# Performance work log

Measured on AMD Instinct MI355X. Metric: run time of the kernel, lower is better.

## Reference

```python
import jax, jax.numpy as jnp
import numpy as np

EMBED_DIM = 1024
NUM_HEADS = 16
HEAD_DIM = EMBED_DIM // NUM_HEADS
SCALE = HEAD_DIM ** -0.5


def setup_inputs() -> dict:
    key = jax.random.key(0)
    k_x, k_qkv_w, k_qkv_b, k_p_w, k_p_b = jax.random.split(key, 5)
    B, N, C = 4, 2048, EMBED_DIM
    std = C ** -0.5
    return {
        "x": jax.random.normal(k_x, (B, N, C), dtype=jnp.float32),
        "qkv_w": jax.random.normal(k_qkv_w, (C, 3 * C), dtype=jnp.float32) * std,
        "qkv_b": jax.random.normal(k_qkv_b, (3 * C,), dtype=jnp.float32) * 0.02,
        "proj_w": jax.random.normal(k_p_w, (C, C), dtype=jnp.float32) * std,
        "proj_b": jax.random.normal(k_p_b, (C,), dtype=jnp.float32) * 0.02,
    }


def reference(x, qkv_w, qkv_b, proj_w, proj_b):
    B, N, C = x.shape
    H, D = NUM_HEADS, HEAD_DIM
    # fused QKV projection: [B, N, 3C] -> [3, B, H, N, D]
    qkv = (x @ qkv_w + qkv_b).reshape(B, N, 3, H, D).transpose(2, 0, 3, 1, 4)
    q, k, v = qkv[0], qkv[1], qkv[2]
    # explicit N x N attention (faithful to the original, no fused SDPA)
    attn = jnp.einsum("bhqd,bhkd->bhqk", q, k) * SCALE
    attn = jax.nn.softmax(attn, axis=-1)
    out = jnp.einsum("bhqk,bhkd->bhqd", attn, v)  # [B, H, N, D]
    out = out.transpose(0, 2, 1, 3).reshape(B, N, C)
    return out @ proj_w + proj_b
```

## Files before the change

### kernel.cpp

```cpp
#include <hip/hip_runtime.h>
#include <hip/hip_bf16.h>

typedef __bf16 bf16x8 __attribute__((ext_vector_type(8)));
typedef __bf16 bf16x4 __attribute__((ext_vector_type(4)));
typedef float  f32x4  __attribute__((ext_vector_type(4)));

#define MFMA_BF16(a, b, c) __builtin_amdgcn_mfma_f32_16x16x32_bf16((a), (b), (c), 0, 0, 0)

typedef const __attribute__((address_space(1))) void* gas_ptr;
typedef __attribute__((address_space(3))) void* las_ptr;

__device__ __forceinline__ void gload_lds16(const void* g, void* l) {
    __builtin_amdgcn_global_load_lds((gas_ptr)g, (las_ptr)l, 16, 0, 0);
}

#define LOG2E 1.44269504088896f
#define QSCALE 0.1803368801111204f

__global__ __launch_bounds__(256) void cvt_f32_bf16(const float* __restrict__ in,
                                                    __bf16* __restrict__ out, int n4) {
    int i = blockIdx.x * 256 + threadIdx.x;
    if (i < n4) {
        float4 v = ((const float4*)in)[i];
        bf16x4 o = {(__bf16)v.x, (__bf16)v.y, (__bf16)v.z, (__bf16)v.w};
        ((bf16x4*)out)[i] = o;
    }
}

__global__ __launch_bounds__(256) void transpose_cvt(const float* __restrict__ in,
                                                     __bf16* __restrict__ out, int R, int C) {
    __shared__ float t[32][33];
    int bx = blockIdx.x * 32, by = blockIdx.y * 32;
    int x = bx + threadIdx.x;
    for (int j = threadIdx.y; j < 32; j += 8)
        t[j][threadIdx.x] = in[(size_t)(by + j) * C + x];
    __syncthreads();
    int x2 = by + threadIdx.x;
    for (int j = threadIdx.y; j < 32; j += 8)
        out[(size_t)(bx + j) * R + x2] = (__bf16)t[threadIdx.x][j];
}

template <int MODE>
__global__ __launch_bounds__(256) void gemm_bt(const __bf16* __restrict__ A,
                                               const __bf16* __restrict__ Bt,
                                               const float* __restrict__ bias,
                                               float* __restrict__ outp,
                                               __bf16* __restrict__ Qp,
                                               __bf16* __restrict__ Kp,
                                               __bf16* __restrict__ Vp,
                                               int M, int Nn, int K) {
    __shared__ __align__(16) __bf16 As[128 * 32];
    __shared__ __align__(16) __bf16 Bs[128 * 32];
    const int tid = threadIdx.x, lane = tid & 63, w = tid >> 6;
    const int wr = w >> 1, wc = w & 1;
    const int row0 = blockIdx.y * 128, col0 = blockIdx.x * 128;
    const __bf16* Ag = A + (size_t)row0 * K;
    const __bf16* Bg = Bt + (size_t)col0 * K;
    const int lr = lane >> 2;
    const int lk = (lane & 3) * 8;
    const int frow = lane & 15, fq = lane >> 4;
    f32x4 acc[4][4];
    for (int i = 0; i < 4; ++i)
        for (int j = 0; j < 4; ++j) acc[i][j] = (f32x4)0.f;

    for (int k0 = 0; k0 < K; k0 += 32) {
        __syncthreads();
        for (int it = 0; it < 2; ++it) {
            int ci = 2 * w + it;
            gload_lds16(Ag + (size_t)(ci * 16 + lr) * K + k0 + lk, &As[ci * 512]);
            gload_lds16(Bg + (size_t)(ci * 16 + lr) * K + k0 + lk, &Bs[ci * 512]);
        }
        __syncthreads();
        bf16x8 af[4], bf[4];
        for (int i = 0; i < 4; ++i)
            af[i] = *(const bf16x8*)&As[(wr * 64 + i * 16 + frow) * 32 + fq * 8];
        for (int j = 0; j < 4; ++j)
            bf[j] = *(const bf16x8*)&Bs[(wc * 64 + j * 16 + frow) * 32 + fq * 8];
        for (int i = 0; i < 4; ++i)
            for (int j = 0; j < 4; ++j) acc[i][j] = MFMA_BF16(af[i], bf[j], acc[i][j]);
    }

    for (int i = 0; i < 4; ++i) {
        int rbase = row0 + wr * 64 + i * 16 + fq * 4;
        for (int j = 0; j < 4; ++j) {
            int c = col0 + wc * 64 + j * 16 + frow;
            float bv = bias[c];
            if (MODE == 0) {
                int which = c >> 10;
                int h = (c >> 6) & 15;
                int d = c & 63;
                if (which == 2) {
                    int b = rbase >> 11, n = rbase & 2047;
                    bf16x4 vv = {(__bf16)(acc[i][j][0] + bv), (__bf16)(acc[i][j][1] + bv),
                                 (__bf16)(acc[i][j][2] + bv), (__bf16)(acc[i][j][3] + bv)};
                    *(bf16x4*)&Vp[(size_t)(((b << 4) + h) * 64 + d) * 2048 + n] = vv;
                } else {
                    for (int rg = 0; rg < 4; ++rg) {
                        int rr = rbase + rg;
                        int b = rr >> 11, n = rr & 2047;
                        float v = acc[i][j][rg] + bv;
                        if (which == 0)
                            Qp[(size_t)(((b << 4) + h) * 2048 + n) * 64 + d] =
                                (__bf16)(v * QSCALE);
                        else
                            Kp[(size_t)(((b << 4) + h) * 2048 + n) * 64 + d] = (__bf16)v;
                    }
                }
            } else {
                for (int rg = 0; rg < 4; ++rg)
                    outp[(size_t)(rbase + rg) * Nn + c] = acc[i][j][rg] + bv;
            }
        }
    }
}

__global__ __launch_bounds__(256, 4) void flash_attn4(const __bf16* __restrict__ Q,
                                                      const __bf16* __restrict__ K,
                                                      const __bf16* __restrict__ Vt,
                                                      __bf16* __restrict__ O) {
    __shared__ __align__(16) __bf16 Kts[2][4096];
    __shared__ __align__(16) __bf16 Vts[2][4096];
    __shared__ __align__(16) __bf16 Ps[4][1024];
    const int tid = threadIdx.x, lane = tid & 63, w = tid >> 6;
    const int frow = lane & 15, fq = lane >> 4;
    const int bh = blockIdx.y;
    const int q0 = blockIdx.x * 128;
    const __bf16* Qg = Q + ((size_t)bh * 2048 + q0 + w * 32) * 64;
    const __bf16* Kb = K + (size_t)bh * 2048 * 64;
    const __bf16* Vb = Vt + (size_t)bh * 64 * 2048;

    bf16x8 qf[2][2];
#pragma unroll
    for (int nt = 0; nt < 2; ++nt)
#pragma unroll
        for (int ks = 0; ks < 2; ++ks)
            qf[nt][ks] = *(const bf16x8*)(Qg + (nt * 16 + frow) * 64 + ks * 32 + fq * 8);

    bf16x8 ones;
#pragma unroll
    for (int i = 0; i < 8; ++i) ones[i] = (__bf16)1.0f;

    f32x4 acc[2][4];
#pragma unroll
    for (int i = 0; i < 2; ++i)
#pragma unroll
        for (int j = 0; j < 4; ++j) acc[i][j] = (f32x4)0.f;
    f32x4 acc_l[2];
#pragma unroll
    for (int i = 0; i < 2; ++i) acc_l[i] = (f32x4)0.f;

    const int s_r16 = lane >> 2;
    const int s_c8 = (lane & 3) * 8;

    auto stage = [&](int kt, int buf) {
#pragma unroll
        for (int it = 0; it < 2; ++it) {
            int ci = 2 * w + it;
            int ks = ci >> 2;
            int r16 = (ci & 3) * 16 + s_r16;
            gload_lds16(Kb + (size_t)(kt * 64 + r16) * 64 + ks * 32 + s_c8,
                        &Kts[buf][ci * 512]);
            gload_lds16(Vb + (size_t)r16 * 2048 + kt * 64 + ks * 32 + s_c8,
                        &Vts[buf][ci * 512]);
        }
    };

    stage(0, 0);

    const int swz = frow & 3;
    const int pe = (fq ^ swz) * 8;
    __bf16* Pw = Ps[w];

    for (int kt = 0; kt < 32; ++kt) {
        const int cur = kt & 1;
        __syncthreads();
        if (kt < 31) stage(kt + 1, cur ^ 1);

        const __bf16* Kc = Kts[cur];
        const __bf16* Vc = Vts[cur];

#pragma unroll
        for (int ph = 0; ph < 2; ++ph) {
#pragma unroll
            for (int mi = 0; mi < 2; ++mi) {
                int mt = ph * 2 + mi;
                bf16x8 a0 = *(const bf16x8*)&Kc[(mt * 16 + frow) * 32 + fq * 8];
                bf16x8 a1 = *(const bf16x8*)&Kc[2048 + (mt * 16 + frow) * 32 + fq * 8];
                f32x4 s[2];
#pragma unroll
                for (int nt = 0; nt < 2; ++nt) {
                    s[nt] = MFMA_BF16(a0, qf[nt][0], (f32x4)0.f);
                    s[nt] = MFMA_BF16(a1, qf[nt][1], s[nt]);
                }
                int u = mi * 2 + (fq >> 1);
                int e = ((u ^ swz) << 3) + ((fq & 1) << 2);
#pragma unroll
                for (int nt = 0; nt < 2; ++nt) {
                    float p0 = __builtin_exp2f(s[nt][0]);
                    float p1 = __builtin_exp2f(s[nt][1]);
                    float p2 = __builtin_exp2f(s[nt][2]);
                    float p3 = __builtin_exp2f(s[nt][3]);
                    bf16x4 pk = {(__bf16)p0, (__bf16)p1, (__bf16)p2, (__bf16)p3};
                    *(bf16x4*)&Pw[(nt * 16 + frow) * 32 + e] = pk;
                }
            }

            bf16x8 vf[4];
#pragma unroll
            for (int nt = 0; nt < 4; ++nt)
                vf[nt] = *(const bf16x8*)&Vc[ph * 2048 + (nt * 16 + frow) * 32 + fq * 8];
#pragma unroll
            for (int mq = 0; mq < 2; ++mq) {
                bf16x8 p = *(const bf16x8*)&Pw[(mq * 16 + frow) * 32 + pe];
#pragma unroll
                for (int nt = 0; nt < 4; ++nt)
                    acc[mq][nt] = MFMA_BF16(p, vf[nt], acc[mq][nt]);
                acc_l[mq] = MFMA_BF16(p, ones, acc_l[mq]);
            }
        }
    }

    const int b = bh >> 4, h = bh & 15;
#pragma unroll
    for (int mq = 0; mq < 2; ++mq)
#pragma unroll
        for (int r = 0; r < 4; ++r) {
            float linv = 1.0f / acc_l[mq][r];
            int qg = q0 + w * 32 + mq * 16 + fq * 4 + r;
            __bf16* orow = O + ((size_t)(b * 2048 + qg)) * 1024 + h * 64 + frow;
#pragma unroll
            for (int nt = 0; nt < 4; ++nt)
                orow[nt * 16] = (__bf16)(acc[mq][nt][r] * linv);
        }
}

extern "C" void kernel_launch(void* const* d_in, const int* in_sizes, int n_in,
                              void* d_out, int out_size, void* d_ws, size_t ws_size,
                              hipStream_t stream) {
    const float* x      = (const float*)d_in[0];
    const float* qkv_w  = (const float*)d_in[1];
    const float* qkv_b  = (const float*)d_in[2];
    const float* proj_w = (const float*)d_in[3];
    const float* proj_b = (const float*)d_in[4];
    float* out = (float*)d_out;

    char* ws = (char*)d_ws;
    __bf16* Xb     = (__bf16*)(ws);
    __bf16* Wqkvt  = (__bf16*)(ws + 16777216);
    __bf16* Wpt    = (__bf16*)(ws + 23068672);
    __bf16* Qb     = (__bf16*)(ws + 25165824);
    __bf16* Kb     = (__bf16*)(ws + 41943040);
    __bf16* Vtb    = (__bf16*)(ws + 58720256);
    __bf16* AttnOut = Xb;

    cvt_f32_bf16<<<8192, 256, 0, stream>>>(x, Xb, 2097152);
    transpose_cvt<<<dim3(96, 32), dim3(32, 8), 0, stream>>>(qkv_w, Wqkvt, 1024, 3072);
    transpose_cvt<<<dim3(32, 32), dim3(32, 8), 0, stream>>>(proj_w, Wpt, 1024, 1024);

    gemm_bt<0><<<dim3(24, 64), 256, 0, stream>>>(Xb, Wqkvt, qkv_b, nullptr,
                                                 Qb, Kb, Vtb, 8192, 3072, 1024);

    flash_attn4<<<dim3(16, 64), 256, 0, stream>>>(Qb, Kb, Vtb, AttnOut);

    gemm_bt<1><<<dim3(8, 64), 256, 0, stream>>>(AttnOut, Wpt, proj_b, out,
                                                nullptr, nullptr, nullptr, 8192, 1024, 1024);
}
```

Measured before the change: 313.3 us.

## Rewrite attention with 32x32 MFMA and register-shuffled P instead of LDS

```diff
diff --git a/kernel.cpp b/kernel.cpp
--- a/kernel.cpp
+++ b/kernel.cpp
@@ -3,9 +3,13 @@
 
 typedef __bf16 bf16x8 __attribute__((ext_vector_type(8)));
 typedef __bf16 bf16x4 __attribute__((ext_vector_type(4)));
+typedef __bf16 bf16x2 __attribute__((ext_vector_type(2)));
 typedef float  f32x4  __attribute__((ext_vector_type(4)));
+typedef float  f32x16 __attribute__((ext_vector_type(16)));
+typedef unsigned uint4v __attribute__((ext_vector_type(4)));
 
 #define MFMA_BF16(a, b, c) __builtin_amdgcn_mfma_f32_16x16x32_bf16((a), (b), (c), 0, 0, 0)
+#define MFMA32(a, b, c) __builtin_amdgcn_mfma_f32_32x32x16_bf16((a), (b), (c), 0, 0, 0)
 
 typedef const __attribute__((address_space(1))) void* gas_ptr;
 typedef __attribute__((address_space(3))) void* las_ptr;
@@ -114,62 +118,54 @@
     }
 }
 
-__global__ __launch_bounds__(256, 4) void flash_attn4(const __bf16* __restrict__ Q,
+__global__ __launch_bounds__(256, 4) void flash_attn5(const __bf16* __restrict__ Q,
                                                       const __bf16* __restrict__ K,
                                                       const __bf16* __restrict__ Vt,
                                                       __bf16* __restrict__ O) {
     __shared__ __align__(16) __bf16 Kts[2][4096];
     __shared__ __align__(16) __bf16 Vts[2][4096];
-    __shared__ __align__(16) __bf16 Ps[4][1024];
     const int tid = threadIdx.x, lane = tid & 63, w = tid >> 6;
-    const int frow = lane & 15, fq = lane >> 4;
+    const int l31 = lane & 31, h = lane >> 5;
     const int bh = blockIdx.y;
     const int q0 = blockIdx.x * 128;
-    const __bf16* Qg = Q + ((size_t)bh * 2048 + q0 + w * 32) * 64;
     const __bf16* Kb = K + (size_t)bh * 2048 * 64;
     const __bf16* Vb = Vt + (size_t)bh * 64 * 2048;
 
-    bf16x8 qf[2][2];
-#pragma unroll
-    for (int nt = 0; nt < 2; ++nt)
-#pragma unroll
-        for (int ks = 0; ks < 2; ++ks)
-            qf[nt][ks] = *(const bf16x8*)(Qg + (nt * 16 + frow) * 64 + ks * 32 + fq * 8);
+    const __bf16* Qg = Q + ((size_t)bh * 2048 + q0 + w * 32 + l31) * 64;
+    bf16x8 qf[4];
+#pragma unroll
+    for (int c = 0; c < 4; ++c)
+        qf[c] = *(const bf16x8*)(Qg + c * 16 + h * 8);
 
     bf16x8 ones;
 #pragma unroll
     for (int i = 0; i < 8; ++i) ones[i] = (__bf16)1.0f;
 
-    f32x4 acc[2][4];
-#pragma unroll
-    for (int i = 0; i < 2; ++i)
-#pragma unroll
-        for (int j = 0; j < 4; ++j) acc[i][j] = (f32x4)0.f;
-    f32x4 acc_l[2];
-#pragma unroll
-    for (int i = 0; i < 2; ++i) acc_l[i] = (f32x4)0.f;
-
-    const int s_r16 = lane >> 2;
-    const int s_c8 = (lane & 3) * 8;
+    f32x16 acc[2];
+    acc[0] = (f32x16)0.f;
+    acc[1] = (f32x16)0.f;
+    f32x16 accl = (f32x16)0.f;
+
+    const int key = l31 & 7;
+    int koff[4];
+#pragma unroll
+    for (int c = 0; c < 4; ++c) koff[c] = ((2 * c + h) ^ key) * 8;
+    const int rbase = l31 * 64;
 
     auto stage = [&](int kt, int buf) {
 #pragma unroll
         for (int it = 0; it < 2; ++it) {
             int ci = 2 * w + it;
-            int ks = ci >> 2;
-            int r16 = (ci & 3) * 16 + s_r16;
-            gload_lds16(Kb + (size_t)(kt * 64 + r16) * 64 + ks * 32 + s_c8,
+            int rloc = ci * 8 + (lane >> 3);
+            int ulog = (lane & 7) ^ (lane >> 3);
+            gload_lds16(Kb + (size_t)(kt * 64 + rloc) * 64 + ulog * 8,
                         &Kts[buf][ci * 512]);
-            gload_lds16(Vb + (size_t)r16 * 2048 + kt * 64 + ks * 32 + s_c8,
+            gload_lds16(Vb + (size_t)rloc * 2048 + kt * 64 + ulog * 8,
                         &Vts[buf][ci * 512]);
         }
     };
 
     stage(0, 0);
-
-    const int swz = frow & 3;
-    const int pe = (fq ^ swz) * 8;
-    __bf16* Pw = Ps[w];
 
     for (int kt = 0; kt < 32; ++kt) {
         const int cur = kt & 1;
@@ -180,58 +176,50 @@
         const __bf16* Vc = Vts[cur];
 
 #pragma unroll
-        for (int ph = 0; ph < 2; ++ph) {
-#pragma unroll
-            for (int mi = 0; mi < 2; ++mi) {
-                int mt = ph * 2 + mi;
-                bf16x8 a0 = *(const bf16x8*)&Kc[(mt * 16 + frow) * 32 + fq * 8];
-                bf16x8 a1 = *(const bf16x8*)&Kc[2048 + (mt * 16 + frow) * 32 + fq * 8];
-                f32x4 s[2];
-#pragma unroll
-                for (int nt = 0; nt < 2; ++nt) {
-                    s[nt] = MFMA_BF16(a0, qf[nt][0], (f32x4)0.f);
-                    s[nt] = MFMA_BF16(a1, qf[nt][1], s[nt]);
+        for (int T = 0; T < 2; ++T) {
+            f32x16 sacc = (f32x16)0.f;
+#pragma unroll
+            for (int c = 0; c < 4; ++c) {
+                bf16x8 kf = *(const bf16x8*)&Kc[T * 2048 + rbase + koff[c]];
+                sacc = MFMA32(kf, qf[c], sacc);
+            }
+            unsigned pk[8];
+#pragma unroll
+            for (int r2 = 0; r2 < 8; ++r2) {
+                bf16x2 pp = {(__bf16)__builtin_exp2f(sacc[2 * r2]),
+                             (__bf16)__builtin_exp2f(sacc[2 * r2 + 1])};
+                pk[r2] = __builtin_bit_cast(unsigned, pp);
+            }
+#pragma unroll
+            for (int cc = 0; cc < 2; ++cc) {
+                unsigned tA = h ? pk[4 * cc] : pk[4 * cc + 2];
+                unsigned tB = h ? pk[4 * cc + 1] : pk[4 * cc + 3];
+                unsigned rA = (unsigned)__shfl_xor((int)tA, 32, 64);
+                unsigned rB = (unsigned)__shfl_xor((int)tB, 32, 64);
+                uint4v fu = {h ? rA : pk[4 * cc], h ? rB : pk[4 * cc + 1],
+                             h ? pk[4 * cc + 2] : rA, h ? pk[4 * cc + 3] : rB};
+                bf16x8 fragP = __builtin_bit_cast(bf16x8, fu);
+                const int cg = T * 2 + cc;
+#pragma unroll
+                for (int t = 0; t < 2; ++t) {
+                    bf16x8 vf = *(const bf16x8*)&Vc[t * 2048 + rbase + koff[cg]];
+                    acc[t] = MFMA32(fragP, vf, acc[t]);
                 }
-                int u = mi * 2 + (fq >> 1);
-                int e = ((u ^ swz) << 3) + ((fq & 1) << 2);
-#pragma unroll
-                for (int nt = 0; nt < 2; ++nt) {
-                    float p0 = __builtin_exp2f(s[nt][0]);
-                    float p1 = __builtin_exp2f(s[nt][1]);
-                    float p2 = __builtin_exp2f(s[nt][2]);
-                    float p3 = __builtin_exp2f(s[nt][3]);
-                    bf16x4 pk = {(__bf16)p0, (__bf16)p1, (__bf16)p2, (__bf16)p3};
-                    *(bf16x4*)&Pw[(nt * 16 + frow) * 32 + e] = pk;
-                }
-            }
-
-            bf16x8 vf[4];
-#pragma unroll
-            for (int nt = 0; nt < 4; ++nt)
-                vf[nt] = *(const bf16x8*)&Vc[ph * 2048 + (nt * 16 + frow) * 32 + fq * 8];
-#pragma unroll
-            for (int mq = 0; mq < 2; ++mq) {
-                bf16x8 p = *(const bf16x8*)&Pw[(mq * 16 + frow) * 32 + pe];
-#pragma unroll
-                for (int nt = 0; nt < 4; ++nt)
-                    acc[mq][nt] = MFMA_BF16(p, vf[nt], acc[mq][nt]);
-                acc_l[mq] = MFMA_BF16(p, ones, acc_l[mq]);
-            }
-        }
-    }
-
-    const int b = bh >> 4, h = bh & 15;
-#pragma unroll
-    for (int mq = 0; mq < 2; ++mq)
-#pragma unroll
-        for (int r = 0; r < 4; ++r) {
-            float linv = 1.0f / acc_l[mq][r];
-            int qg = q0 + w * 32 + mq * 16 + fq * 4 + r;
-            __bf16* orow = O + ((size_t)(b * 2048 + qg)) * 1024 + h * 64 + frow;
-#pragma unroll
-            for (int nt = 0; nt < 4; ++nt)
-                orow[nt * 16] = (__bf16)(acc[mq][nt][r] * linv);
-        }
+                accl = MFMA32(fragP, ones, accl);
+            }
+        }
+    }
+
+    const int b = bh >> 4, hd = bh & 15;
+#pragma unroll
+    for (int reg = 0; reg < 16; ++reg) {
+        int qloc = (reg & 3) + 8 * (reg >> 2) + 4 * h;
+        int qg = q0 + w * 32 + qloc;
+        float linv = 1.0f / accl[reg];
+        __bf16* orow = O + ((size_t)(b * 2048 + qg)) * 1024 + hd * 64;
+        orow[l31] = (__bf16)(acc[0][reg] * linv);
+        orow[32 + l31] = (__bf16)(acc[1][reg] * linv);
+    }
 }
 
 extern "C" void kernel_launch(void* const* d_in, const int* in_sizes, int n_in,
@@ -260,7 +248,7 @@
     gemm_bt<0><<<dim3(24, 64), 256, 0, stream>>>(Xb, Wqkvt, qkv_b, nullptr,
                                                  Qb, Kb, Vtb, 8192, 3072, 1024);
 
-    flash_attn4<<<dim3(16, 64), 256, 0, stream>>>(Qb, Kb, Vtb, AttnOut);
+    flash_attn5<<<dim3(16, 64), 256, 0, stream>>>(Qb, Kb, Vtb, AttnOut);
 
     gemm_bt<1><<<dim3(8, 64), 256, 0, stream>>>(AttnOut, Wpt, proj_b, out,
                                                 nullptr, nullptr, nullptr, 8192, 1024, 1024);
```

Measured after the change: 316.9 us. Within noise of the previous version (+1.1%).
